# Performance work log

Measured on AMD Instinct MI355X. Metric: run time of the kernel, lower is better.

## Reference

```python
import jax, jax.numpy as jnp
import numpy as np

DIM = 64
SQRT_DIM = np.sqrt(DIM).astype(np.float32)
NEG_INF = -1e9


def setup_inputs() -> dict:
    key = jax.random.key(0)
    kq, kk, kv, km = jax.random.split(key, 4)
    B, Q, K, D = 32, 1024, 1024, DIM
    query = jax.random.normal(kq, (B, Q, D), dtype=jnp.float32)
    k = jax.random.normal(kk, (B, K, D), dtype=jnp.float32)
    value = jax.random.normal(kv, (B, K, D), dtype=jnp.float32)
    mask = jax.random.randint(km, (B, Q, K), 0, 2).astype(jnp.bool_)
    return {"query": query, "key": k, "value": value, "mask": mask}


def reference(query, key, value, mask):
    # score: [B, Q, K]
    score = jnp.einsum('bqd,bkd->bqk', query, key) / SQRT_DIM
    score = jnp.where(mask, NEG_INF, score)
    attn = jax.nn.softmax(score, axis=-1)
    context = jnp.einsum('bqk,bkd->bqd', attn, value)
    return (context, attn)
```

## Files before the change

kernel.cpp:

```cpp
#include <hip/hip_runtime.h>

constexpr int BATCH = 32;
constexpr int QLEN  = 1024;
constexpr int KLEN  = 1024;
constexpr int DIM   = 64;
constexpr int TQ    = 16;

typedef float    f32x4 __attribute__((ext_vector_type(4)));
typedef int      i32x4 __attribute__((ext_vector_type(4)));
typedef _Float16 f16x8 __attribute__((ext_vector_type(8)));
typedef _Float16 f16x4 __attribute__((ext_vector_type(4)));
typedef unsigned long long u64;
typedef unsigned int u32;

__device__ __forceinline__ f16x8 cvt_h8(f32x4 a, f32x4 b) {
  f16x8 h;
  h[0] = (_Float16)a[0]; h[1] = (_Float16)a[1]; h[2] = (_Float16)a[2]; h[3] = (_Float16)a[3];
  h[4] = (_Float16)b[0]; h[5] = (_Float16)b[1]; h[6] = (_Float16)b[2]; h[7] = (_Float16)b[3];
  return h;
}

constexpr int TK = 128;
__global__ __launch_bounds__(256)
void vtkh_kernel(const float* __restrict__ V, const float* __restrict__ Kg,
                 _Float16* __restrict__ Vt, _Float16* __restrict__ Kh) {
  __shared__ _Float16 lt[DIM][TK + 8];
  const int b = blockIdx.y, k0 = blockIdx.x * TK;
  const int t = threadIdx.x;
  const int d4 = (t & 15) * 4;
  #pragma unroll
  for (int p = 0; p < TK / 16; ++p) {
    const int kl = (t >> 4) + p * 16;
    const f32x4 v = *(const f32x4*)(V + ((size_t)(b * KLEN + k0 + kl)) * DIM + d4);
    #pragma unroll
    for (int j = 0; j < 4; ++j) lt[d4 + j][kl] = (_Float16)v[j];
  }
  #pragma unroll
  for (int p = 0; p < 8; ++p) {
    const int idx = t + p * 256;
    const int kl = idx >> 4, dd = (idx & 15) * 4;
    const f32x4 v = *(const f32x4*)(Kg + ((size_t)(b * KLEN + k0 + kl)) * DIM + dd);
    f16x4 h = { (_Float16)v[0], (_Float16)v[1], (_Float16)v[2], (_Float16)v[3] };
    *(f16x4*)(Kh + ((size_t)(b * KLEN + k0 + kl)) * DIM + dd) = h;
  }
  __syncthreads();
  const int d = t >> 2;
  #pragma unroll
  for (int j2 = 0; j2 < TK / 32; ++j2) {
    const int seg = (t & 3) + j2 * 4;
    *(f16x8*)(Vt + (size_t)b * DIM * KLEN + (size_t)d * KLEN + k0 + seg * 8) =
        *(const f16x8*)(&lt[d][seg * 8]);
  }
}

__global__ __launch_bounds__(256, 4)
void sdpa_kernel(const float* __restrict__ Qg, const _Float16* __restrict__ Kh,
                 const _Float16* __restrict__ Vt, const int* __restrict__ Mg,
                 float* __restrict__ Ctx, float* __restrict__ Attn)
{
  __shared__ float rs[4][16];
  __shared__ __attribute__((aligned(16))) _Float16 sp[TQ * 1024];

  const int tid  = threadIdx.x;
  const int w    = tid >> 6;
  const int l    = tid & 63;
  const int n16  = l & 15;
  const int quad = l >> 4;
  char* const spb = (char*)sp;

  const int lin  = blockIdx.x;
  const int nlin = (lin & 7) * (BATCH * (QLEN / TQ) / 8) + (lin >> 3);
  const int b    = nlin >> 6;
  const int q0   = (nlin & 63) * TQ;

  const float qscl = 0.125f * 1.44269504f;
  const float* qb = Qg + ((size_t)(b * QLEN + q0 + n16)) * DIM + quad * 8;
  f32x4 qa0 = *(const f32x4*)(qb),      qa1 = *(const f32x4*)(qb + 4);
  f32x4 qa2 = *(const f32x4*)(qb + 32), qa3 = *(const f32x4*)(qb + 36);
  #pragma unroll
  for (int i = 0; i < 4; ++i) { qa0[i] *= qscl; qa1[i] *= qscl; qa2[i] *= qscl; qa3[i] *= qscl; }
  const f16x8 aq0 = cvt_h8(qa0, qa1);
  const f16x8 aq1 = cvt_h8(qa2, qa3);

  const _Float16* kb = Kh + (size_t)b * KLEN * DIM + quad * 8;
  const int* mrow = Mg + ((size_t)(b * QLEN + q0 + n16)) * KLEN + w * 256 + quad * 4;

  f32x4 rsum4 = {0.f, 0.f, 0.f, 0.f};
  f16x4 ec[16];
  #pragma unroll
  for (int tt = 0; tt < 16; ++tt) {
    const i32x4 mv = *(const i32x4*)(mrow + tt * 16);
    const _Float16* kp = kb + (size_t)((w * 16 + tt) * 16 + n16) * DIM;
    const f16x8 ak0 = *(const f16x8*)(kp);
    const f16x8 ak1 = *(const f16x8*)(kp + 32);
    f32x4 acc = {0.f, 0.f, 0.f, 0.f};
    acc = __builtin_amdgcn_mfma_f32_16x16x32_f16(ak0, aq0, acc, 0, 0, 0);
    acc = __builtin_amdgcn_mfma_f32_16x16x32_f16(ak1, aq1, acc, 0, 0, 0);
    f32x4 e;
    #pragma unroll
    for (int i = 0; i < 4; ++i) {
      e[i] = mv[i] ? 0.f : __builtin_amdgcn_exp2f(acc[i]);
      rsum4[i] += e[i];
    }
    ec[tt] = f16x4{ (_Float16)e[0], (_Float16)e[1], (_Float16)e[2], (_Float16)e[3] };
  }
  float rsum = (rsum4[0] + rsum4[1]) + (rsum4[2] + rsum4[3]);
  rsum += __shfl_xor(rsum, 16, 64);
  rsum += __shfl_xor(rsum, 32, 64);
  if (quad == 0) rs[w][n16] = rsum;
  __syncthreads();
  const float inv =
      __builtin_amdgcn_rcpf(rs[0][n16] + rs[1][n16] + rs[2][n16] + rs[3][n16]);

  #pragma unroll
  for (int tt = 0; tt < 16; ++tt) {
    f32x4 ev;
    #pragma unroll
    for (int i = 0; i < 4; ++i) ev[i] = (float)ec[tt][i] * inv;
    f16x4 ph = { (_Float16)ev[0], (_Float16)ev[1], (_Float16)ev[2], (_Float16)ev[3] };
    const int g = w * 64 + tt * 4 + quad;
    *(f16x4*)(spb + (n16 << 11) + ((g * 8) ^ ((n16 & 7) << 4))) = ph;
  }
  __syncthreads();

  #pragma unroll
  for (int rr = 0; rr < 4; ++rr) {
    const int row = w * 4 + rr;
    float* arow = Attn + ((size_t)(b * QLEN + q0 + row)) * KLEN;
    #pragma unroll
    for (int j = 0; j < 4; ++j) {
      const int g = j * 64 + l;
      const f16x4 hv = *(const f16x4*)(spb + (row << 11) + ((g * 8) ^ ((row & 7) << 4)));
      f32x4 ov = { (float)hv[0], (float)hv[1], (float)hv[2], (float)hv[3] };
      __builtin_nontemporal_store(ov, (f32x4*)(arow + j * 256 + l * 4));
    }
  }

  const _Float16* vtb = Vt + ((size_t)(b * DIM + w * 16 + n16)) * KLEN;
  f32x4 c0 = {0.f, 0.f, 0.f, 0.f}, c1 = {0.f, 0.f, 0.f, 0.f};
  #pragma unroll 8
  for (int m = 0; m < 32; m += 2) {
    const int ga = m * 8 + quad * 2;
    const f16x8 pa0 = *(const f16x8*)(spb + (n16 << 11) + ((ga * 8) ^ ((n16 & 7) << 4)));
    const f16x8 pa1 = *(const f16x8*)(spb + (n16 << 11) + (((ga + 8) * 8) ^ ((n16 & 7) << 4)));
    const f16x8 bv0 = *(const f16x8*)(vtb + m * 32 + quad * 8);
    const f16x8 bv1 = *(const f16x8*)(vtb + (m + 1) * 32 + quad * 8);
    c0 = __builtin_amdgcn_mfma_f32_16x16x32_f16(bv0, pa0, c0, 0, 0, 0);
    c1 = __builtin_amdgcn_mfma_f32_16x16x32_f16(bv1, pa1, c1, 0, 0, 0);
  }
  f32x4 cv = { c0[0] + c1[0], c0[1] + c1[1], c0[2] + c1[2], c0[3] + c1[3] };
  *(f32x4*)(Ctx + ((size_t)(b * QLEN + q0 + n16)) * DIM + w * 16 + quad * 4) = cv;
}

extern "C" void kernel_launch(void* const* d_in, const int* in_sizes, int n_in,
                              void* d_out, int out_size, void* d_ws, size_t ws_size,
                              hipStream_t stream) {
  const float* Qg = (const float*)d_in[0];
  const float* Kg = (const float*)d_in[1];
  const float* Vg = (const float*)d_in[2];
  const int*   Mg = (const int*)d_in[3];
  float* Ctx  = (float*)d_out;
  float* Attn = (float*)d_out + (size_t)BATCH * QLEN * DIM;
  _Float16* Vt = (_Float16*)d_ws;
  _Float16* Kh = (_Float16*)((char*)d_ws + (size_t)BATCH * DIM * KLEN * 2);

  dim3 tgrid(KLEN / TK, BATCH);
  vtkh_kernel<<<tgrid, 256, 0, stream>>>(Vg, Kg, Vt, Kh);

  sdpa_kernel<<<2048, 256, 0, stream>>>(Qg, Kh, Vt, Mg, Ctx, Attn);
}
```

Baseline: 306.1 us.

## Split softmax row-sum pass into separate kernel with bit-packed mask

Adds a score kernel that reads the int mask, computes QK^T and the exp row sums, and writes the row sums plus a packed 64-bit mask per thread to workspace. The main kernel then recomputes QK^T, normalises directly using the precomputed row sum, and drops the in-block reduction barrier and the ec register array. The intent is to cut register pressure and the mask read inside the main kernel, at the cost of an extra launch and computing QK^T and exp twice.

Result: slower. 336.5 us (+9.9%).

```diff
diff --git a/kernel.cpp b/kernel.cpp
--- a/kernel.cpp
+++ b/kernel.cpp
@@ -18,6 +18,12 @@
   h[0] = (_Float16)a[0]; h[1] = (_Float16)a[1]; h[2] = (_Float16)a[2]; h[3] = (_Float16)a[3];
   h[4] = (_Float16)b[0]; h[5] = (_Float16)b[1]; h[6] = (_Float16)b[2]; h[7] = (_Float16)b[3];
   return h;
+}
+
+__device__ __forceinline__ void block_map(int lin, int& b, int& q0) {
+  const int nlin = (lin & 7) * (BATCH * (QLEN / TQ) / 8) + (lin >> 3);
+  b  = nlin >> 6;
+  q0 = (nlin & 63) * TQ;
 }
 
 constexpr int TK = 128;
@@ -53,12 +59,66 @@
   }
 }
 
+__global__ __launch_bounds__(256)
+void score_kernel(const float* __restrict__ Qg, const _Float16* __restrict__ Kh,
+                  const int* __restrict__ Mg, u64* __restrict__ Mp,
+                  float* __restrict__ Rs)
+{
+  __shared__ float rs[4][16];
+  const int tid  = threadIdx.x;
+  const int w    = tid >> 6;
+  const int l    = tid & 63;
+  const int n16  = l & 15;
+  const int quad = l >> 4;
+  int b, q0; block_map(blockIdx.x, b, q0);
+
+  const float qscl = 0.125f * 1.44269504f;
+  const float* qb = Qg + ((size_t)(b * QLEN + q0 + n16)) * DIM + quad * 8;
+  f32x4 qa0 = *(const f32x4*)(qb),      qa1 = *(const f32x4*)(qb + 4);
+  f32x4 qa2 = *(const f32x4*)(qb + 32), qa3 = *(const f32x4*)(qb + 36);
+  #pragma unroll
+  for (int i = 0; i < 4; ++i) { qa0[i] *= qscl; qa1[i] *= qscl; qa2[i] *= qscl; qa3[i] *= qscl; }
+  const f16x8 aq0 = cvt_h8(qa0, qa1);
+  const f16x8 aq1 = cvt_h8(qa2, qa3);
+
+  const _Float16* kb = Kh + (size_t)b * KLEN * DIM + quad * 8;
+  const int* mrow = Mg + ((size_t)(b * QLEN + q0 + n16)) * KLEN + w * 256 + quad * 4;
+
+  f32x4 rsum4 = {0.f, 0.f, 0.f, 0.f};
+  u64 pm = 0;
+  #pragma unroll
+  for (int tt = 0; tt < 16; ++tt) {
+    const i32x4 mv = __builtin_nontemporal_load((const i32x4*)(mrow + tt * 16));
+    const _Float16* kp = kb + (size_t)((w * 16 + tt) * 16 + n16) * DIM;
+    const f16x8 ak0 = *(const f16x8*)(kp);
+    const f16x8 ak1 = *(const f16x8*)(kp + 32);
+    f32x4 acc = {0.f, 0.f, 0.f, 0.f};
+    acc = __builtin_amdgcn_mfma_f32_16x16x32_f16(ak0, aq0, acc, 0, 0, 0);
+    acc = __builtin_amdgcn_mfma_f32_16x16x32_f16(ak1, aq1, acc, 0, 0, 0);
+    #pragma unroll
+    for (int i = 0; i < 4; ++i) {
+      const bool msk = (mv[i] != 0);
+      pm |= (u64)(msk ? 1u : 0u) << (tt * 4 + i);
+      rsum4[i] += msk ? 0.f : __builtin_amdgcn_exp2f(acc[i]);
+    }
+  }
+  Mp[(size_t)blockIdx.x * 256 + tid] = pm;
+
+  float rsum = (rsum4[0] + rsum4[1]) + (rsum4[2] + rsum4[3]);
+  rsum += __shfl_xor(rsum, 16, 64);
+  rsum += __shfl_xor(rsum, 32, 64);
+  if (quad == 0) rs[w][n16] = rsum;
+  __syncthreads();
+  if (tid < 16)
+    Rs[(size_t)b * QLEN + q0 + tid] = rs[0][tid] + rs[1][tid] + rs[2][tid] + rs[3][tid];
+}
+
 __global__ __launch_bounds__(256, 4)
 void sdpa_kernel(const float* __restrict__ Qg, const _Float16* __restrict__ Kh,
-                 const _Float16* __restrict__ Vt, const int* __restrict__ Mg,
+                 const _Float16* __restrict__ Vt, const u64* __restrict__ Mp,
+                 const float* __restrict__ Rs,
                  float* __restrict__ Ctx, float* __restrict__ Attn)
 {
-  __shared__ float rs[4][16];
   __shared__ __attribute__((aligned(16))) _Float16 sp[TQ * 1024];
 
   const int tid  = threadIdx.x;
@@ -67,11 +127,7 @@
   const int n16  = l & 15;
   const int quad = l >> 4;
   char* const spb = (char*)sp;
-
-  const int lin  = blockIdx.x;
-  const int nlin = (lin & 7) * (BATCH * (QLEN / TQ) / 8) + (lin >> 3);
-  const int b    = nlin >> 6;
-  const int q0   = (nlin & 63) * TQ;
+  int b, q0; block_map(blockIdx.x, b, q0);
 
   const float qscl = 0.125f * 1.44269504f;
   const float* qb = Qg + ((size_t)(b * QLEN + q0 + n16)) * DIM + quad * 8;
@@ -82,42 +138,26 @@
   const f16x8 aq0 = cvt_h8(qa0, qa1);
   const f16x8 aq1 = cvt_h8(qa2, qa3);
 
+  const u64 pm = Mp[(size_t)blockIdx.x * 256 + tid];
+  const float inv = __builtin_amdgcn_rcpf(Rs[(size_t)b * QLEN + q0 + n16]);
+
   const _Float16* kb = Kh + (size_t)b * KLEN * DIM + quad * 8;
-  const int* mrow = Mg + ((size_t)(b * QLEN + q0 + n16)) * KLEN + w * 256 + quad * 4;
-
-  f32x4 rsum4 = {0.f, 0.f, 0.f, 0.f};
-  f16x4 ec[16];
+
   #pragma unroll
   for (int tt = 0; tt < 16; ++tt) {
-    const i32x4 mv = *(const i32x4*)(mrow + tt * 16);
     const _Float16* kp = kb + (size_t)((w * 16 + tt) * 16 + n16) * DIM;
     const f16x8 ak0 = *(const f16x8*)(kp);
     const f16x8 ak1 = *(const f16x8*)(kp + 32);
     f32x4 acc = {0.f, 0.f, 0.f, 0.f};
     acc = __builtin_amdgcn_mfma_f32_16x16x32_f16(ak0, aq0, acc, 0, 0, 0);
     acc = __builtin_amdgcn_mfma_f32_16x16x32_f16(ak1, aq1, acc, 0, 0, 0);
-    f32x4 e;
+    f16x4 ph;
     #pragma unroll
     for (int i = 0; i < 4; ++i) {
-      e[i] = mv[i] ? 0.f : __builtin_amdgcn_exp2f(acc[i]);
-      rsum4[i] += e[i];
+      const float e = ((pm >> (tt * 4 + i)) & 1ULL) ? 0.f
+                        : __builtin_amdgcn_exp2f(acc[i]) * inv;
+      ph[i] = (_Float16)e;
     }
-    ec[tt] = f16x4{ (_Float16)e[0], (_Float16)e[1], (_Float16)e[2], (_Float16)e[3] };
-  }
-  float rsum = (rsum4[0] + rsum4[1]) + (rsum4[2] + rsum4[3]);
-  rsum += __shfl_xor(rsum, 16, 64);
-  rsum += __shfl_xor(rsum, 32, 64);
-  if (quad == 0) rs[w][n16] = rsum;
-  __syncthreads();
-  const float inv =
-      __builtin_amdgcn_rcpf(rs[0][n16] + rs[1][n16] + rs[2][n16] + rs[3][n16]);
-
-  #pragma unroll
-  for (int tt = 0; tt < 16; ++tt) {
-    f32x4 ev;
-    #pragma unroll
-    for (int i = 0; i < 4; ++i) ev[i] = (float)ec[tt][i] * inv;
-    f16x4 ph = { (_Float16)ev[0], (_Float16)ev[1], (_Float16)ev[2], (_Float16)ev[3] };
     const int g = w * 64 + tt * 4 + quad;
     *(f16x4*)(spb + (n16 << 11) + ((g * 8) ^ ((n16 & 7) << 4))) = ph;
   }
@@ -161,11 +201,17 @@
   const int*   Mg = (const int*)d_in[3];
   float* Ctx  = (float*)d_out;
   float* Attn = (float*)d_out + (size_t)BATCH * QLEN * DIM;
-  _Float16* Vt = (_Float16*)d_ws;
-  _Float16* Kh = (_Float16*)((char*)d_ws + (size_t)BATCH * DIM * KLEN * 2);
+
+  char* ws = (char*)d_ws;
+  _Float16* Vt = (_Float16*)ws;
+  _Float16* Kh = (_Float16*)(ws + (size_t)4 * 1024 * 1024);
+  u64*      Mp = (u64*)     (ws + (size_t)8 * 1024 * 1024);
+  float*    Rs = (float*)   (ws + (size_t)12 * 1024 * 1024);
 
   dim3 tgrid(KLEN / TK, BATCH);
   vtkh_kernel<<<tgrid, 256, 0, stream>>>(Vg, Kg, Vt, Kh);
 
-  sdpa_kernel<<<2048, 256, 0, stream>>>(Qg, Kh, Vt, Mg, Ctx, Attn);
-}
+  score_kernel<<<2048, 256, 0, stream>>>(Qg, Kh, Mg, Mp, Rs);
+
+  sdpa_kernel<<<2048, 256, 0, stream>>>(Qg, Kh, Vt, Mp, Rs, Ctx, Attn);
+}
```
